# Kernel optimization log

Measured on AMD Instinct MI355X. Metric: run time of the kernel, lower is better.

The kernel has to match this reference:

```python
import jax, jax.numpy as jnp
import numpy as np

B, L, H, E = 8, 1024, 8, 64
HIST = 512


def setup_inputs() -> dict:
    key = jax.random.key(0)
    ks = jax.random.split(key, 6)
    shp = (B, L, H, E)
    q, k, v, qd, kd, vd = (jax.random.normal(kk, shp, dtype=jnp.float32) for kk in ks)
    # DoubleTriangularCausalMask surrogate: strictly-upper-triangular causal mask (diagonal=1)
    attn_mask = jnp.triu(jnp.ones((L, L), dtype=bool), k=1)[None, None]  # (1,1,L,S)
    return {
        "queries": q, "keys": k, "values": v,
        "queries_drawn": qd, "keys_drawn": kd, "values_drawn": vd,
        "attn_mask": attn_mask, "history_len": HIST,
    }


def reference(queries, keys, values, queries_drawn, keys_drawn, values_drawn, attn_mask, history_len):
    # drawn_y=True branch of FullFixedTimeCausalConstructiveAttention with history_len set.
    B, L, H, E = queries.shape
    scale = 1.0 / float(np.sqrt(E))
    hist = history_len
    idx = jnp.arange(hist, L)

    # queries[:, hist:] = queries_drawn[:, hist:]
    q_eff = jnp.concatenate([queries[:, :hist], queries_drawn[:, hist:]], axis=1)

    scores = jnp.einsum('blhe,bshe->bhls', q_eff, keys)  # (B,H,L,S)
    # diagonal positions l>=hist use drawn keys: q_eff[l] . keys_drawn[l]
    diag_scores = jnp.einsum('blhe,blhe->bhl', q_eff[:, hist:], keys_drawn[:, hist:])
    scores = scores.at[:, :, idx, idx].set(diag_scores)

    scores = jnp.where(attn_mask, -jnp.inf, scores)
    A = jax.nn.softmax(scale * scores, axis=-1)  # (B,H,L,S); dropout rate 0 in eval

    # values substitution on the diagonal (l==s, l>=hist) is a rank-1 correction;
    # avoids materializing the torch (B,H,D,L,S) repeated tensor.
    V = jnp.einsum('bhls,bshd->blhd', A, values)
    diag_A = A[:, :, idx, idx]                      # (B,H,L-hist)
    delta = values_drawn[:, hist:] - values[:, hist:]  # (B,L-hist,H,D)
    V = V.at[:, hist:].add(jnp.transpose(diag_A, (0, 2, 1))[..., None] * delta)
    return V
```

## Files before the change

### kernel.cpp

```cpp
#include <hip/hip_runtime.h>

#define LL   1024
#define HH   8
#define EE   64
#define KSTR 72

#define SCALE2 0.18033688011112043f

typedef _Float16 f16;
typedef _Float16 v8h  __attribute__((ext_vector_type(8)));
typedef _Float16 h2   __attribute__((ext_vector_type(2)));
typedef float    v4f  __attribute__((ext_vector_type(4)));
typedef int      v2i  __attribute__((ext_vector_type(2)));

__device__ __forceinline__ float fexp2(float x) {
#if __has_builtin(__builtin_amdgcn_exp2f)
  return __builtin_amdgcn_exp2f(x);
#else
  return __expf(x * 0.6931471805599453f);
#endif
}

__device__ __forceinline__ h2 pkh2(float a, float b) {
#if __has_builtin(__builtin_amdgcn_cvt_pkrtz)
  return __builtin_bit_cast(h2, __builtin_amdgcn_cvt_pkrtz(a, b));
#else
  h2 r; r[0] = (f16)a; r[1] = (f16)b; return r;
#endif
}

__device__ __forceinline__ float red4max(float x) {
#if __has_builtin(__builtin_amdgcn_permlane16_swap) && __has_builtin(__builtin_amdgcn_permlane32_swap)
  int xi = __float_as_int(x);
  v2i a = __builtin_amdgcn_permlane16_swap(xi, xi, false, false);
  float m = fmaxf(__int_as_float(a.x), __int_as_float(a.y));
  int mi = __float_as_int(m);
  v2i b = __builtin_amdgcn_permlane32_swap(mi, mi, false, false);
  return fmaxf(__int_as_float(b.x), __int_as_float(b.y));
#else
  x = fmaxf(x, __shfl_xor(x, 16));
  return fmaxf(x, __shfl_xor(x, 32));
#endif
}

__device__ __forceinline__ float red4sum(float x) {
#if __has_builtin(__builtin_amdgcn_permlane16_swap) && __has_builtin(__builtin_amdgcn_permlane32_swap)
  int xi = __float_as_int(x);
  v2i a = __builtin_amdgcn_permlane16_swap(xi, xi, false, false);
  float s = __int_as_float(a.x) + __int_as_float(a.y);
  int si = __float_as_int(s);
  v2i b = __builtin_amdgcn_permlane32_swap(si, si, false, false);
  return __int_as_float(b.x) + __int_as_float(b.y);
#else
  x += __shfl_xor(x, 16);
  return x + __shfl_xor(x, 32);
#endif
}

__device__ __forceinline__ void load16f(const float* __restrict__ p, float* __restrict__ f) {
  const float4* p4 = reinterpret_cast<const float4*>(p);
  float4 a = p4[0], b = p4[1], c = p4[2], d = p4[3];
  f[0]=a.x;  f[1]=a.y;  f[2]=a.z;  f[3]=a.w;
  f[4]=b.x;  f[5]=b.y;  f[6]=b.z;  f[7]=b.w;
  f[8]=c.x;  f[9]=c.y;  f[10]=c.z; f[11]=c.w;
  f[12]=d.x; f[13]=d.y; f[14]=d.z; f[15]=d.w;
}

__device__ __forceinline__ void load8f(const float* __restrict__ p, float* __restrict__ f) {
  const float4* p4 = reinterpret_cast<const float4*>(p);
  float4 a = p4[0], b = p4[1];
  f[0]=a.x; f[1]=a.y; f[2]=a.z; f[3]=a.w;
  f[4]=b.x; f[5]=b.y; f[6]=b.z; f[7]=b.w;
}

struct TileState {
  v4f   o[4];
  float m, l, pd;
};

__device__ __forceinline__ void tile_update(
    TileState& st, const v8h* __restrict__ qf, bool dt, bool drawn,
    const f16* __restrict__ Ks, const f16* __restrict__ Vt,
    const float* __restrict__ zd,
    int w, int ln, int lq,
    const int* __restrict__ rk, const int* __restrict__ kb)
{
  v4f S[4];
#pragma unroll
  for (int nb = 0; nb < 4; ++nb) {
    const f16* krow = &Ks[rk[nb] * KSTR + 8 * lq];
    v8h k0 = *reinterpret_cast<const v8h*>(krow);
    v8h k1 = *reinterpret_cast<const v8h*>(krow + 32);
    v4f acc = (v4f){0.f, 0.f, 0.f, 0.f};
    acc = __builtin_amdgcn_mfma_f32_16x16x32_f16(k0, qf[0], acc, 0, 0, 0);
    acc = __builtin_amdgcn_mfma_f32_16x16x32_f16(k1, qf[1], acc, 0, 0, 0);
    S[nb] = acc;
  }

  float z[4][4];
#pragma unroll
  for (int nb = 0; nb < 4; ++nb)
#pragma unroll
    for (int r = 0; r < 4; ++r) z[nb][r] = S[nb][r] * SCALE2;

  const int qlocal = w * 16 + ln;
  if (dt) {
    const float zdq = drawn ? zd[qlocal] : 0.f;
#pragma unroll
    for (int nb = 0; nb < 4; ++nb) {
#pragma unroll
      for (int r = 0; r < 4; ++r) {
        const int kl = kb[nb] + r;
        if (kl > qlocal)                 z[nb][r] = -1e30f;
        else if (drawn && kl == qlocal)  z[nb][r] = zdq;
      }
    }
  }

  float a0 = fmaxf(fmaxf(z[0][0], z[0][1]), fmaxf(z[0][2], z[0][3]));
  float a1 = fmaxf(fmaxf(z[1][0], z[1][1]), fmaxf(z[1][2], z[1][3]));
  float a2 = fmaxf(fmaxf(z[2][0], z[2][1]), fmaxf(z[2][2], z[2][3]));
  float a3 = fmaxf(fmaxf(z[3][0], z[3][1]), fmaxf(z[3][2], z[3][3]));
  const float mx = red4max(fmaxf(fmaxf(a0, a1), fmaxf(a2, a3)));

  const float mn = fmaxf(st.m, mx);
  const float al = fexp2(st.m - mn);
  st.m = mn;

  float p[4][4], rsum = 0.f, pdl = 0.f;
#pragma unroll
  for (int nb = 0; nb < 4; ++nb) {
#pragma unroll
    for (int r = 0; r < 4; ++r) {
      const float pv = fexp2(z[nb][r] - mn);
      p[nb][r] = pv;
      rsum += pv;
      if (dt && drawn && (kb[nb] + r) == qlocal) pdl = pv;
    }
  }
  rsum = red4sum(rsum);
  if (dt && drawn) st.pd = red4sum(pdl);
  st.l = st.l * al + rsum;
#pragma unroll
  for (int nb = 0; nb < 4; ++nb)
#pragma unroll
    for (int r = 0; r < 4; ++r) st.o[nb][r] *= al;

  h2 wq[4][2];
#pragma unroll
  for (int nb = 0; nb < 4; ++nb) {
    wq[nb][0] = pkh2(p[nb][0], p[nb][1]);
    wq[nb][1] = pkh2(p[nb][2], p[nb][3]);
  }
  const bool swp = (lq & 1);
  union U8 { v8h v; h2 h[4]; } A0, A1;
  A0.h[0] = swp ? wq[1][0] : wq[0][0];
  A0.h[1] = swp ? wq[1][1] : wq[0][1];
  A0.h[2] = swp ? wq[0][0] : wq[1][0];
  A0.h[3] = swp ? wq[0][1] : wq[1][1];
  A1.h[0] = swp ? wq[3][0] : wq[2][0];
  A1.h[1] = swp ? wq[3][1] : wq[2][1];
  A1.h[2] = swp ? wq[2][0] : wq[3][0];
  A1.h[3] = swp ? wq[2][1] : wq[3][1];

#pragma unroll
  for (int nb = 0; nb < 4; ++nb) {
    const int d   = nb * 16 + ln;
    const int dsw = (d >> 3) & 7;
    const f16* vbase = &Vt[d * KSTR];
    v8h v0 = *reinterpret_cast<const v8h*>(vbase + (((lq    ) ^ dsw) & 7) * 8);
    v8h v1 = *reinterpret_cast<const v8h*>(vbase + (((lq + 4) ^ dsw) & 7) * 8);
    st.o[nb] = __builtin_amdgcn_mfma_f32_16x16x32_f16(v0, A0.v, st.o[nb], 0, 0, 0);
    st.o[nb] = __builtin_amdgcn_mfma_f32_16x16x32_f16(v1, A1.v, st.o[nb], 0, 0, 0);
  }
}

extern "C" __global__ __launch_bounds__(256, 4)
void ftcca_split(const float* __restrict__ Q,  const float* __restrict__ K,
                 const float* __restrict__ V,  const float* __restrict__ Qd,
                 const float* __restrict__ Kd, const float* __restrict__ Vd,
                 float* __restrict__ out)
{
  __shared__ f16   Ks[64 * KSTR];
  __shared__ f16   Vt[64 * KSTR];
  __shared__ float zdiag[64];

  const int bh  = blockIdx.x & 63;
  const int a   = blockIdx.x >> 6;
  const int qt  = 15 - a;
  const bool drawn = (qt >= 8);
  const int b   = bh >> 3, h = bh & 7;
  const int t   = threadIdx.x;
  const int w    = t >> 6;
  const int lane = t & 63;
  const int ln   = lane & 15;
  const int lq   = lane >> 4;
  const int rs   = t >> 2;
  const int es0  = (t & 3) * 16;
  const int vr0  = (t >> 3) * 2;
  const int vd0  = (t & 7) * 8;

  const size_t base = ((size_t)b * LL * HH + h) * EE;
  const int ROWF = HH * EE;

  const int q2 = ln >> 2;
  int rk[4], kb[4];
  rk[0] = ln + ((q2 + 1) >> 1) * 8;
  rk[1] = ln + 4 + (q2 >> 1) * 8;
  rk[2] = rk[0] + 32;
  rk[3] = rk[1] + 32;
  kb[0] = 4 * lq + ((lq + 1) >> 1) * 8;
  kb[1] = 4 * lq + 4 + (lq >> 1) * 8;
  kb[2] = kb[0] + 32;
  kb[3] = kb[1] + 32;

  if (drawn) {
    const int l = qt * 64 + rs;
    const float* qrow = Qd + base + (size_t)l * ROWF + es0;
    const float* krow = Kd + base + (size_t)l * ROWF + es0;
    float par = 0.f;
#pragma unroll
    for (int i = 0; i < 16; ++i) par += qrow[i] * krow[i];
    par += __shfl_xor(par, 1);
    par += __shfl_xor(par, 2);
    if ((t & 3) == 0) zdiag[rs] = SCALE2 * par;
  }

  const int rowt_q = w * 16 + ln;
  const float* qsrc = drawn ? Qd : Q;
  v8h qf[2];
  {
    const float* pq = qsrc + base + (size_t)(qt * 64 + rowt_q) * ROWF;
#pragma unroll
    for (int c = 0; c < 2; ++c) {
      const float* x = pq + 32 * c + 8 * lq;
#pragma unroll
      for (int j = 0; j < 8; ++j) qf[c][j] = (f16)x[j];
    }
  }

  TileState st;
#pragma unroll
  for (int nb = 0; nb < 4; ++nb) st.o[nb] = (v4f){0, 0, 0, 0};
  st.m = -1e30f; st.l = 0.f; st.pd = 0.f;

  float tk[16], tv[16];
  load16f(K + base + (size_t)rs * ROWF + es0, tk);
  load8f(V + base + (size_t)vr0 * ROWF + vd0, tv);
  load8f(V + base + (size_t)(vr0 + 1) * ROWF + vd0, tv + 8);

  for (int i = 0; i <= qt; ++i) {
    __syncthreads();
    {
      v8h k0, k1;
#pragma unroll
      for (int j = 0; j < 8; ++j) { k0[j] = (f16)tk[j]; k1[j] = (f16)tk[8 + j]; }
      v8h* kd0 = reinterpret_cast<v8h*>(&Ks[rs * KSTR + es0]);
      kd0[0] = k0;
      kd0[1] = k1;
      const int vswz = vr0 >> 3;
#pragma unroll
      for (int dd = 0; dd < 8; ++dd) {
        const int d  = vd0 + dd;
        const int ch = (vswz ^ (d >> 3)) & 7;
        h2 val; val[0] = (f16)tv[dd]; val[1] = (f16)tv[8 + dd];
        *reinterpret_cast<h2*>(&Vt[d * KSTR + ch * 8 + (vr0 & 7)]) = val;
      }
    }
    __syncthreads();

    if (i < qt) {
      const size_t r0 = (size_t)((i + 1) * 64);
      load16f(K + base + (r0 + rs) * ROWF + es0, tk);
      load8f(V + base + (r0 + vr0) * ROWF + vd0, tv);
      load8f(V + base + (r0 + vr0 + 1) * ROWF + vd0, tv + 8);
    }

    tile_update(st, qf, i == qt, drawn, Ks, Vt, zdiag, w, ln, lq, rk, kb);
  }

  const float inv = 1.f / st.l;
  const float pdinv = st.pd * inv;
  const int lrow = qt * 64 + w * 16 + ln;

#pragma unroll
  for (int nb = 0; nb < 4; ++nb) {
    const int d0 = nb * 16 + lq * 4;
    const size_t g = base + (size_t)lrow * ROWF + d0;
    float4 o4;
    o4.x = st.o[nb][0] * inv;
    o4.y = st.o[nb][1] * inv;
    o4.z = st.o[nb][2] * inv;
    o4.w = st.o[nb][3] * inv;
    if (drawn) {
      float4 vd4 = *reinterpret_cast<const float4*>(Vd + g);
      float4 v4  = *reinterpret_cast<const float4*>(V + g);
      o4.x += pdinv * (vd4.x - v4.x);
      o4.y += pdinv * (vd4.y - v4.y);
      o4.z += pdinv * (vd4.z - v4.z);
      o4.w += pdinv * (vd4.w - v4.w);
    }
    *reinterpret_cast<float4*>(out + g) = o4;
  }
}

extern "C" void kernel_launch(void* const* d_in, const int* in_sizes, int n_in,
                              void* d_out, int out_size, void* d_ws, size_t ws_size,
                              hipStream_t stream) {
  const float* q  = (const float*)d_in[0];
  const float* k  = (const float*)d_in[1];
  const float* v  = (const float*)d_in[2];
  const float* qd = (const float*)d_in[3];
  const float* kd = (const float*)d_in[4];
  const float* vd = (const float*)d_in[5];
  float* out = (float*)d_out;

  ftcca_split<<<dim3(1024), dim3(256), 0, stream>>>(q, k, v, qd, kd, vd, out);
}
```

Before: 155.5 us.

## Pair mirrored causal query tiles per block to share K/V staging

Each block now processes two query tiles, a drawn tile 15-a and a history tile a, so the total causal work per block is balanced. The K/V tiles loaded into shared memory are reused by both tiles, which halves global loads and conversions and halves the grid size. The register footprint roughly doubles, so launch bounds drop to 2 blocks per SM, which lowers occupancy and may limit latency hiding.

```diff
diff --git a/kernel.cpp b/kernel.cpp
--- a/kernel.cpp
+++ b/kernel.cpp
@@ -12,6 +12,8 @@
 typedef _Float16 h2   __attribute__((ext_vector_type(2)));
 typedef float    v4f  __attribute__((ext_vector_type(4)));
 typedef int      v2i  __attribute__((ext_vector_type(2)));
+
+union U8 { v8h v; h2 h[4]; };
 
 __device__ __forceinline__ float fexp2(float x) {
 #if __has_builtin(__builtin_amdgcn_exp2f)
@@ -78,34 +80,17 @@
   float m, l, pd;
 };
 
-__device__ __forceinline__ void tile_update(
-    TileState& st, const v8h* __restrict__ qf, bool dt, bool drawn,
-    const f16* __restrict__ Ks, const f16* __restrict__ Vt,
-    const float* __restrict__ zd,
-    int w, int ln, int lq,
-    const int* __restrict__ rk, const int* __restrict__ kb)
+__device__ __forceinline__ void softmax_pack(
+    TileState& st, const v4f* __restrict__ S, bool dt, bool drawn, float zdq,
+    int qlocal, const int* __restrict__ kb, int lq, U8& A0, U8& A1)
 {
-  v4f S[4];
-#pragma unroll
-  for (int nb = 0; nb < 4; ++nb) {
-    const f16* krow = &Ks[rk[nb] * KSTR + 8 * lq];
-    v8h k0 = *reinterpret_cast<const v8h*>(krow);
-    v8h k1 = *reinterpret_cast<const v8h*>(krow + 32);
-    v4f acc = (v4f){0.f, 0.f, 0.f, 0.f};
-    acc = __builtin_amdgcn_mfma_f32_16x16x32_f16(k0, qf[0], acc, 0, 0, 0);
-    acc = __builtin_amdgcn_mfma_f32_16x16x32_f16(k1, qf[1], acc, 0, 0, 0);
-    S[nb] = acc;
-  }
-
   float z[4][4];
 #pragma unroll
   for (int nb = 0; nb < 4; ++nb)
 #pragma unroll
     for (int r = 0; r < 4; ++r) z[nb][r] = S[nb][r] * SCALE2;
 
-  const int qlocal = w * 16 + ln;
   if (dt) {
-    const float zdq = drawn ? zd[qlocal] : 0.f;
 #pragma unroll
     for (int nb = 0; nb < 4; ++nb) {
 #pragma unroll
@@ -153,7 +138,6 @@
     wq[nb][1] = pkh2(p[nb][2], p[nb][3]);
   }
   const bool swp = (lq & 1);
-  union U8 { v8h v; h2 h[4]; } A0, A1;
   A0.h[0] = swp ? wq[1][0] : wq[0][0];
   A0.h[1] = swp ? wq[1][1] : wq[0][1];
   A0.h[2] = swp ? wq[0][0] : wq[1][0];
@@ -162,21 +146,10 @@
   A1.h[1] = swp ? wq[3][1] : wq[2][1];
   A1.h[2] = swp ? wq[2][0] : wq[3][0];
   A1.h[3] = swp ? wq[2][1] : wq[3][1];
-
-#pragma unroll
-  for (int nb = 0; nb < 4; ++nb) {
-    const int d   = nb * 16 + ln;
-    const int dsw = (d >> 3) & 7;
-    const f16* vbase = &Vt[d * KSTR];
-    v8h v0 = *reinterpret_cast<const v8h*>(vbase + (((lq    ) ^ dsw) & 7) * 8);
-    v8h v1 = *reinterpret_cast<const v8h*>(vbase + (((lq + 4) ^ dsw) & 7) * 8);
-    st.o[nb] = __builtin_amdgcn_mfma_f32_16x16x32_f16(v0, A0.v, st.o[nb], 0, 0, 0);
-    st.o[nb] = __builtin_amdgcn_mfma_f32_16x16x32_f16(v1, A1.v, st.o[nb], 0, 0, 0);
-  }
-}
-
-extern "C" __global__ __launch_bounds__(256, 4)
-void ftcca_split(const float* __restrict__ Q,  const float* __restrict__ K,
+}
+
+extern "C" __global__ __launch_bounds__(256, 2)
+void ftcca_pair2(const float* __restrict__ Q,  const float* __restrict__ K,
                  const float* __restrict__ V,  const float* __restrict__ Qd,
                  const float* __restrict__ Kd, const float* __restrict__ Vd,
                  float* __restrict__ out)
@@ -187,8 +160,8 @@
 
   const int bh  = blockIdx.x & 63;
   const int a   = blockIdx.x >> 6;
-  const int qt  = 15 - a;
-  const bool drawn = (qt >= 8);
+  const int qtA = 15 - a;
+  const int qtB = a;
   const int b   = bh >> 3, h = bh & 7;
   const int t   = threadIdx.x;
   const int w    = t >> 6;
@@ -214,8 +187,8 @@
   kb[2] = kb[0] + 32;
   kb[3] = kb[1] + 32;
 
-  if (drawn) {
-    const int l = qt * 64 + rs;
+  {
+    const int l = qtA * 64 + rs;
     const float* qrow = Qd + base + (size_t)l * ROWF + es0;
     const float* krow = Kd + base + (size_t)l * ROWF + es0;
     float par = 0.f;
@@ -227,29 +200,33 @@
   }
 
   const int rowt_q = w * 16 + ln;
-  const float* qsrc = drawn ? Qd : Q;
-  v8h qf[2];
+  v8h qfA[2], qfB[2];
   {
-    const float* pq = qsrc + base + (size_t)(qt * 64 + rowt_q) * ROWF;
+    const float* pa = Qd + base + (size_t)(qtA * 64 + rowt_q) * ROWF;
+    const float* pb = Q  + base + (size_t)(qtB * 64 + rowt_q) * ROWF;
 #pragma unroll
     for (int c = 0; c < 2; ++c) {
-      const float* x = pq + 32 * c + 8 * lq;
-#pragma unroll
-      for (int j = 0; j < 8; ++j) qf[c][j] = (f16)x[j];
-    }
-  }
-
-  TileState st;
-#pragma unroll
-  for (int nb = 0; nb < 4; ++nb) st.o[nb] = (v4f){0, 0, 0, 0};
-  st.m = -1e30f; st.l = 0.f; st.pd = 0.f;
+      const float* xa = pa + 32 * c + 8 * lq;
+      const float* xb = pb + 32 * c + 8 * lq;
+#pragma unroll
+      for (int j = 0; j < 8; ++j) { qfA[c][j] = (f16)xa[j]; qfB[c][j] = (f16)xb[j]; }
+    }
+  }
+
+  TileState stA, stB;
+#pragma unroll
+  for (int nb = 0; nb < 4; ++nb) { stA.o[nb] = (v4f){0,0,0,0}; stB.o[nb] = (v4f){0,0,0,0}; }
+  stA.m = -1e30f; stA.l = 0.f; stA.pd = 0.f;
+  stB.m = -1e30f; stB.l = 0.f; stB.pd = 0.f;
+
+  const int qlocal = w * 16 + ln;
 
   float tk[16], tv[16];
   load16f(K + base + (size_t)rs * ROWF + es0, tk);
   load8f(V + base + (size_t)vr0 * ROWF + vd0, tv);
   load8f(V + base + (size_t)(vr0 + 1) * ROWF + vd0, tv + 8);
 
-  for (int i = 0; i <= qt; ++i) {
+  for (int i = 0; i <= qtA; ++i) {
     __syncthreads();
     {
       v8h k0, k1;
@@ -269,38 +246,97 @@
     }
     __syncthreads();
 
-    if (i < qt) {
+    if (i < qtA) {
       const size_t r0 = (size_t)((i + 1) * 64);
       load16f(K + base + (r0 + rs) * ROWF + es0, tk);
       load8f(V + base + (r0 + vr0) * ROWF + vd0, tv);
       load8f(V + base + (r0 + vr0 + 1) * ROWF + vd0, tv + 8);
     }
 
-    tile_update(st, qf, i == qt, drawn, Ks, Vt, zdiag, w, ln, lq, rk, kb);
-  }
-
-  const float inv = 1.f / st.l;
-  const float pdinv = st.pd * inv;
-  const int lrow = qt * 64 + w * 16 + ln;
-
-#pragma unroll
-  for (int nb = 0; nb < 4; ++nb) {
-    const int d0 = nb * 16 + lq * 4;
-    const size_t g = base + (size_t)lrow * ROWF + d0;
-    float4 o4;
-    o4.x = st.o[nb][0] * inv;
-    o4.y = st.o[nb][1] * inv;
-    o4.z = st.o[nb][2] * inv;
-    o4.w = st.o[nb][3] * inv;
-    if (drawn) {
+    const bool doB = (i <= qtB);
+    const bool dtA = (i == qtA);
+    const bool dtB = (i == qtB);
+
+    v8h k0f[4], k1f[4];
+#pragma unroll
+    for (int nb = 0; nb < 4; ++nb) {
+      const f16* krow = &Ks[rk[nb] * KSTR + 8 * lq];
+      k0f[nb] = *reinterpret_cast<const v8h*>(krow);
+      k1f[nb] = *reinterpret_cast<const v8h*>(krow + 32);
+    }
+
+    v4f SA[4], SB[4];
+#pragma unroll
+    for (int nb = 0; nb < 4; ++nb) {
+      v4f acc = (v4f){0.f, 0.f, 0.f, 0.f};
+      acc = __builtin_amdgcn_mfma_f32_16x16x32_f16(k0f[nb], qfA[0], acc, 0, 0, 0);
+      acc = __builtin_amdgcn_mfma_f32_16x16x32_f16(k1f[nb], qfA[1], acc, 0, 0, 0);
+      SA[nb] = acc;
+    }
+    if (doB) {
+#pragma unroll
+      for (int nb = 0; nb < 4; ++nb) {
+        v4f acc = (v4f){0.f, 0.f, 0.f, 0.f};
+        acc = __builtin_amdgcn_mfma_f32_16x16x32_f16(k0f[nb], qfB[0], acc, 0, 0, 0);
+        acc = __builtin_amdgcn_mfma_f32_16x16x32_f16(k1f[nb], qfB[1], acc, 0, 0, 0);
+        SB[nb] = acc;
+      }
+    }
+
+    U8 pA0, pA1, pB0, pB1;
+    const float zdq = dtA ? zdiag[qlocal] : 0.f;
+    softmax_pack(stA, SA, dtA, true,  zdq, qlocal, kb, lq, pA0, pA1);
+    if (doB)
+      softmax_pack(stB, SB, dtB, false, 0.f, qlocal, kb, lq, pB0, pB1);
+
+#pragma unroll
+    for (int nb = 0; nb < 4; ++nb) {
+      const int d   = nb * 16 + ln;
+      const int dsw = (d >> 3) & 7;
+      const f16* vbase = &Vt[d * KSTR];
+      v8h v0 = *reinterpret_cast<const v8h*>(vbase + (((lq    ) ^ dsw) & 7) * 8);
+      v8h v1 = *reinterpret_cast<const v8h*>(vbase + (((lq + 4) ^ dsw) & 7) * 8);
+      stA.o[nb] = __builtin_amdgcn_mfma_f32_16x16x32_f16(v0, pA0.v, stA.o[nb], 0, 0, 0);
+      stA.o[nb] = __builtin_amdgcn_mfma_f32_16x16x32_f16(v1, pA1.v, stA.o[nb], 0, 0, 0);
+      if (doB) {
+        stB.o[nb] = __builtin_amdgcn_mfma_f32_16x16x32_f16(v0, pB0.v, stB.o[nb], 0, 0, 0);
+        stB.o[nb] = __builtin_amdgcn_mfma_f32_16x16x32_f16(v1, pB1.v, stB.o[nb], 0, 0, 0);
+      }
+    }
+  }
+
+  {
+    const float inv = 1.f / stA.l;
+    const float pdinv = stA.pd * inv;
+    const int lrow = qtA * 64 + w * 16 + ln;
+#pragma unroll
+    for (int nb = 0; nb < 4; ++nb) {
+      const int d0 = nb * 16 + lq * 4;
+      const size_t g = base + (size_t)lrow * ROWF + d0;
       float4 vd4 = *reinterpret_cast<const float4*>(Vd + g);
       float4 v4  = *reinterpret_cast<const float4*>(V + g);
-      o4.x += pdinv * (vd4.x - v4.x);
-      o4.y += pdinv * (vd4.y - v4.y);
-      o4.z += pdinv * (vd4.z - v4.z);
-      o4.w += pdinv * (vd4.w - v4.w);
-    }
-    *reinterpret_cast<float4*>(out + g) = o4;
+      float4 o4;
+      o4.x = stA.o[nb][0] * inv + pdinv * (vd4.x - v4.x);
+      o4.y = stA.o[nb][1] * inv + pdinv * (vd4.y - v4.y);
+      o4.z = stA.o[nb][2] * inv + pdinv * (vd4.z - v4.z);
+      o4.w = stA.o[nb][3] * inv + pdinv * (vd4.w - v4.w);
+      *reinterpret_cast<float4*>(out + g) = o4;
+    }
+  }
+  {
+    const float inv = 1.f / stB.l;
+    const int lrow = qtB * 64 + w * 16 + ln;
+#pragma unroll
+    for (int nb = 0; nb < 4; ++nb) {
+      const int d0 = nb * 16 + lq * 4;
+      const size_t g = base + (size_t)lrow * ROWF + d0;
+      float4 o4;
+      o4.x = stB.o[nb][0] * inv;
+      o4.y = stB.o[nb][1] * inv;
+      o4.z = stB.o[nb][2] * inv;
+      o4.w = stB.o[nb][3] * inv;
+      *reinterpret_cast<float4*>(out + g) = o4;
+    }
   }
 }
 
@@ -315,5 +351,5 @@
   const float* vd = (const float*)d_in[5];
   float* out = (float*)d_out;
 
-  ftcca_split<<<dim3(1024), dim3(256), 0, stream>>>(q, k, v, qd, kd, vd, out);
-}
+  ftcca_pair2<<<dim3(512), dim3(256), 0, stream>>>(q, k, v, qd, kd, vd, out);
+}
```

Measured after the change: 151.0 us. 1.03x faster.

## Double-buffer K/V shared-memory tiles to halve barriers per iteration

Applied to the files above, without the earlier changes.

Splits the K and V LDS tiles into two buffers. Each iteration writes the next tile into the alternate buffer while computing on the current one, so only one __syncthreads is needed per iteration instead of two, and the global prefetch runs two tiles ahead. This doubles LDS use per block (about 37KB), which may limit occupancy under launch_bounds(256,4), and keeps the prefetch registers live during compute.

```diff
diff --git a/kernel.cpp b/kernel.cpp
--- a/kernel.cpp
+++ b/kernel.cpp
@@ -176,13 +176,13 @@
 }
 
 extern "C" __global__ __launch_bounds__(256, 4)
-void ftcca_split(const float* __restrict__ Q,  const float* __restrict__ K,
-                 const float* __restrict__ V,  const float* __restrict__ Qd,
-                 const float* __restrict__ Kd, const float* __restrict__ Vd,
-                 float* __restrict__ out)
+void ftcca_dbuf(const float* __restrict__ Q,  const float* __restrict__ K,
+                const float* __restrict__ V,  const float* __restrict__ Qd,
+                const float* __restrict__ Kd, const float* __restrict__ Vd,
+                float* __restrict__ out)
 {
-  __shared__ f16   Ks[64 * KSTR];
-  __shared__ f16   Vt[64 * KSTR];
+  __shared__ f16   Ks[2][64 * KSTR];
+  __shared__ f16   Vt[2][64 * KSTR];
   __shared__ float zdiag[64];
 
   const int bh  = blockIdx.x & 63;
@@ -244,39 +244,63 @@
   for (int nb = 0; nb < 4; ++nb) st.o[nb] = (v4f){0, 0, 0, 0};
   st.m = -1e30f; st.l = 0.f; st.pd = 0.f;
 
+  const int iters = qt + 1;
+  const int vswz = vr0 >> 3;
+
   float tk[16], tv[16];
   load16f(K + base + (size_t)rs * ROWF + es0, tk);
   load8f(V + base + (size_t)vr0 * ROWF + vd0, tv);
   load8f(V + base + (size_t)(vr0 + 1) * ROWF + vd0, tv + 8);
-
-  for (int i = 0; i <= qt; ++i) {
-    __syncthreads();
-    {
+  {
+    v8h k0, k1;
+#pragma unroll
+    for (int j = 0; j < 8; ++j) { k0[j] = (f16)tk[j]; k1[j] = (f16)tk[8 + j]; }
+    v8h* kd0 = reinterpret_cast<v8h*>(&Ks[0][rs * KSTR + es0]);
+    kd0[0] = k0;
+    kd0[1] = k1;
+#pragma unroll
+    for (int dd = 0; dd < 8; ++dd) {
+      const int d  = vd0 + dd;
+      const int ch = (vswz ^ (d >> 3)) & 7;
+      h2 val; val[0] = (f16)tv[dd]; val[1] = (f16)tv[8 + dd];
+      *reinterpret_cast<h2*>(&Vt[0][d * KSTR + ch * 8 + (vr0 & 7)]) = val;
+    }
+  }
+  if (iters > 1) {
+    const size_t r0 = 64;
+    load16f(K + base + (r0 + rs) * ROWF + es0, tk);
+    load8f(V + base + (r0 + vr0) * ROWF + vd0, tv);
+    load8f(V + base + (r0 + vr0 + 1) * ROWF + vd0, tv + 8);
+  }
+  __syncthreads();
+
+  for (int i = 0; i < iters; ++i) {
+    if (i + 1 < iters) {
+      f16* Kw = Ks[(i + 1) & 1];
+      f16* Vw = Vt[(i + 1) & 1];
       v8h k0, k1;
 #pragma unroll
       for (int j = 0; j < 8; ++j) { k0[j] = (f16)tk[j]; k1[j] = (f16)tk[8 + j]; }
-      v8h* kd0 = reinterpret_cast<v8h*>(&Ks[rs * KSTR + es0]);
+      v8h* kd0 = reinterpret_cast<v8h*>(&Kw[rs * KSTR + es0]);
       kd0[0] = k0;
       kd0[1] = k1;
-      const int vswz = vr0 >> 3;
 #pragma unroll
       for (int dd = 0; dd < 8; ++dd) {
         const int d  = vd0 + dd;
         const int ch = (vswz ^ (d >> 3)) & 7;
         h2 val; val[0] = (f16)tv[dd]; val[1] = (f16)tv[8 + dd];
-        *reinterpret_cast<h2*>(&Vt[d * KSTR + ch * 8 + (vr0 & 7)]) = val;
+        *reinterpret_cast<h2*>(&Vw[d * KSTR + ch * 8 + (vr0 & 7)]) = val;
       }
-    }
+      if (i + 2 < iters) {
+        const size_t r0 = (size_t)((i + 2) * 64);
+        load16f(K + base + (r0 + rs) * ROWF + es0, tk);
+        load8f(V + base + (r0 + vr0) * ROWF + vd0, tv);
+        load8f(V + base + (r0 + vr0 + 1) * ROWF + vd0, tv + 8);
+      }
+    }
+
+    tile_update(st, qf, i == qt, drawn, Ks[i & 1], Vt[i & 1], zdiag, w, ln, lq, rk, kb);
     __syncthreads();
-
-    if (i < qt) {
-      const size_t r0 = (size_t)((i + 1) * 64);
-      load16f(K + base + (r0 + rs) * ROWF + es0, tk);
-      load8f(V + base + (r0 + vr0) * ROWF + vd0, tv);
-      load8f(V + base + (r0 + vr0 + 1) * ROWF + vd0, tv + 8);
-    }
-
-    tile_update(st, qf, i == qt, drawn, Ks, Vt, zdiag, w, ln, lq, rk, kb);
   }
 
   const float inv = 1.f / st.l;
@@ -315,5 +339,5 @@
   const float* vd = (const float*)d_in[5];
   float* out = (float*)d_out;
 
-  ftcca_split<<<dim3(1024), dim3(256), 0, stream>>>(q, k, v, qd, kd, vd, out);
-}
+  ftcca_dbuf<<<dim3(1024), dim3(256), 0, stream>>>(q, k, v, qd, kd, vd, out);
+}
```

Measured after the change: 157.5 us. About the same (+1.3%).

## Drop shared-memory staging; load K/V fragments directly from global memory per wave

Applied to the files above, without the earlier changes.

Removes the LDS tiles for K and transposed V along with the two barriers per iteration. Each wave now reads its MFMA K and V fragments straight from global memory and converts them to fp16 in registers. The diagonal drawn score is computed per lane with a cross-lane reduction instead of through shared memory. This trades barrier and LDS overhead for four-fold redundant global/L2 traffic across the waves of a block, strided scalar V loads, and the loss of software prefetch.

```diff
diff --git a/kernel.cpp b/kernel.cpp
--- a/kernel.cpp
+++ b/kernel.cpp
@@ -3,7 +3,6 @@
 #define LL   1024
 #define HH   8
 #define EE   64
-#define KSTR 72
 
 #define SCALE2 0.18033688011112043f
 
@@ -73,118 +72,12 @@
   f[4]=b.x; f[5]=b.y; f[6]=b.z; f[7]=b.w;
 }
 
-struct TileState {
-  v4f   o[4];
-  float m, l, pd;
-};
-
-__device__ __forceinline__ void tile_update(
-    TileState& st, const v8h* __restrict__ qf, bool dt, bool drawn,
-    const f16* __restrict__ Ks, const f16* __restrict__ Vt,
-    const float* __restrict__ zd,
-    int w, int ln, int lq,
-    const int* __restrict__ rk, const int* __restrict__ kb)
-{
-  v4f S[4];
-#pragma unroll
-  for (int nb = 0; nb < 4; ++nb) {
-    const f16* krow = &Ks[rk[nb] * KSTR + 8 * lq];
-    v8h k0 = *reinterpret_cast<const v8h*>(krow);
-    v8h k1 = *reinterpret_cast<const v8h*>(krow + 32);
-    v4f acc = (v4f){0.f, 0.f, 0.f, 0.f};
-    acc = __builtin_amdgcn_mfma_f32_16x16x32_f16(k0, qf[0], acc, 0, 0, 0);
-    acc = __builtin_amdgcn_mfma_f32_16x16x32_f16(k1, qf[1], acc, 0, 0, 0);
-    S[nb] = acc;
-  }
-
-  float z[4][4];
-#pragma unroll
-  for (int nb = 0; nb < 4; ++nb)
-#pragma unroll
-    for (int r = 0; r < 4; ++r) z[nb][r] = S[nb][r] * SCALE2;
-
-  const int qlocal = w * 16 + ln;
-  if (dt) {
-    const float zdq = drawn ? zd[qlocal] : 0.f;
-#pragma unroll
-    for (int nb = 0; nb < 4; ++nb) {
-#pragma unroll
-      for (int r = 0; r < 4; ++r) {
-        const int kl = kb[nb] + r;
-        if (kl > qlocal)                 z[nb][r] = -1e30f;
-        else if (drawn && kl == qlocal)  z[nb][r] = zdq;
-      }
-    }
-  }
-
-  float a0 = fmaxf(fmaxf(z[0][0], z[0][1]), fmaxf(z[0][2], z[0][3]));
-  float a1 = fmaxf(fmaxf(z[1][0], z[1][1]), fmaxf(z[1][2], z[1][3]));
-  float a2 = fmaxf(fmaxf(z[2][0], z[2][1]), fmaxf(z[2][2], z[2][3]));
-  float a3 = fmaxf(fmaxf(z[3][0], z[3][1]), fmaxf(z[3][2], z[3][3]));
-  const float mx = red4max(fmaxf(fmaxf(a0, a1), fmaxf(a2, a3)));
-
-  const float mn = fmaxf(st.m, mx);
-  const float al = fexp2(st.m - mn);
-  st.m = mn;
-
-  float p[4][4], rsum = 0.f, pdl = 0.f;
-#pragma unroll
-  for (int nb = 0; nb < 4; ++nb) {
-#pragma unroll
-    for (int r = 0; r < 4; ++r) {
-      const float pv = fexp2(z[nb][r] - mn);
-      p[nb][r] = pv;
-      rsum += pv;
-      if (dt && drawn && (kb[nb] + r) == qlocal) pdl = pv;
-    }
-  }
-  rsum = red4sum(rsum);
-  if (dt && drawn) st.pd = red4sum(pdl);
-  st.l = st.l * al + rsum;
-#pragma unroll
-  for (int nb = 0; nb < 4; ++nb)
-#pragma unroll
-    for (int r = 0; r < 4; ++r) st.o[nb][r] *= al;
-
-  h2 wq[4][2];
-#pragma unroll
-  for (int nb = 0; nb < 4; ++nb) {
-    wq[nb][0] = pkh2(p[nb][0], p[nb][1]);
-    wq[nb][1] = pkh2(p[nb][2], p[nb][3]);
-  }
-  const bool swp = (lq & 1);
-  union U8 { v8h v; h2 h[4]; } A0, A1;
-  A0.h[0] = swp ? wq[1][0] : wq[0][0];
-  A0.h[1] = swp ? wq[1][1] : wq[0][1];
-  A0.h[2] = swp ? wq[0][0] : wq[1][0];
-  A0.h[3] = swp ? wq[0][1] : wq[1][1];
-  A1.h[0] = swp ? wq[3][0] : wq[2][0];
-  A1.h[1] = swp ? wq[3][1] : wq[2][1];
-  A1.h[2] = swp ? wq[2][0] : wq[3][0];
-  A1.h[3] = swp ? wq[2][1] : wq[3][1];
-
-#pragma unroll
-  for (int nb = 0; nb < 4; ++nb) {
-    const int d   = nb * 16 + ln;
-    const int dsw = (d >> 3) & 7;
-    const f16* vbase = &Vt[d * KSTR];
-    v8h v0 = *reinterpret_cast<const v8h*>(vbase + (((lq    ) ^ dsw) & 7) * 8);
-    v8h v1 = *reinterpret_cast<const v8h*>(vbase + (((lq + 4) ^ dsw) & 7) * 8);
-    st.o[nb] = __builtin_amdgcn_mfma_f32_16x16x32_f16(v0, A0.v, st.o[nb], 0, 0, 0);
-    st.o[nb] = __builtin_amdgcn_mfma_f32_16x16x32_f16(v1, A1.v, st.o[nb], 0, 0, 0);
-  }
-}
-
-extern "C" __global__ __launch_bounds__(256, 4)
-void ftcca_split(const float* __restrict__ Q,  const float* __restrict__ K,
+extern "C" __global__ __launch_bounds__(256)
+void ftcca_nolds(const float* __restrict__ Q,  const float* __restrict__ K,
                  const float* __restrict__ V,  const float* __restrict__ Qd,
                  const float* __restrict__ Kd, const float* __restrict__ Vd,
                  float* __restrict__ out)
 {
-  __shared__ f16   Ks[64 * KSTR];
-  __shared__ f16   Vt[64 * KSTR];
-  __shared__ float zdiag[64];
-
   const int bh  = blockIdx.x & 63;
   const int a   = blockIdx.x >> 6;
   const int qt  = 15 - a;
@@ -195,10 +88,6 @@
   const int lane = t & 63;
   const int ln   = lane & 15;
   const int lq   = lane >> 4;
-  const int rs   = t >> 2;
-  const int es0  = (t & 3) * 16;
-  const int vr0  = (t >> 3) * 2;
-  const int vd0  = (t & 7) * 8;
 
   const size_t base = ((size_t)b * LL * HH + h) * EE;
   const int ROWF = HH * EE;
@@ -214,84 +103,159 @@
   kb[2] = kb[0] + 32;
   kb[3] = kb[1] + 32;
 
+  const int qlocal = w * 16 + ln;
+
+  float zdq = 0.f;
   if (drawn) {
-    const int l = qt * 64 + rs;
-    const float* qrow = Qd + base + (size_t)l * ROWF + es0;
-    const float* krow = Kd + base + (size_t)l * ROWF + es0;
-    float par = 0.f;
-#pragma unroll
-    for (int i = 0; i < 16; ++i) par += qrow[i] * krow[i];
-    par += __shfl_xor(par, 1);
-    par += __shfl_xor(par, 2);
-    if ((t & 3) == 0) zdiag[rs] = SCALE2 * par;
-  }
-
-  const int rowt_q = w * 16 + ln;
+    const int qrow = qt * 64 + qlocal;
+    float fq[16], fk[16];
+    load16f(Qd + base + (size_t)qrow * ROWF + 16 * lq, fq);
+    load16f(Kd + base + (size_t)qrow * ROWF + 16 * lq, fk);
+    float pa = 0.f;
+#pragma unroll
+    for (int ii = 0; ii < 16; ++ii) pa += fq[ii] * fk[ii];
+    zdq = SCALE2 * red4sum(pa);
+  }
+
   const float* qsrc = drawn ? Qd : Q;
   v8h qf[2];
   {
-    const float* pq = qsrc + base + (size_t)(qt * 64 + rowt_q) * ROWF;
+    const float* pq = qsrc + base + (size_t)(qt * 64 + qlocal) * ROWF;
 #pragma unroll
     for (int c = 0; c < 2; ++c) {
-      const float* x = pq + 32 * c + 8 * lq;
+      float x[8];
+      load8f(pq + 32 * c + 8 * lq, x);
 #pragma unroll
       for (int j = 0; j < 8; ++j) qf[c][j] = (f16)x[j];
     }
   }
 
-  TileState st;
-#pragma unroll
-  for (int nb = 0; nb < 4; ++nb) st.o[nb] = (v4f){0, 0, 0, 0};
-  st.m = -1e30f; st.l = 0.f; st.pd = 0.f;
-
-  float tk[16], tv[16];
-  load16f(K + base + (size_t)rs * ROWF + es0, tk);
-  load8f(V + base + (size_t)vr0 * ROWF + vd0, tv);
-  load8f(V + base + (size_t)(vr0 + 1) * ROWF + vd0, tv + 8);
+  v4f   o[4];
+#pragma unroll
+  for (int nb = 0; nb < 4; ++nb) o[nb] = (v4f){0, 0, 0, 0};
+  float m = -1e30f, l = 0.f, pd = 0.f;
 
   for (int i = 0; i <= qt; ++i) {
-    __syncthreads();
-    {
-      v8h k0, k1;
-#pragma unroll
-      for (int j = 0; j < 8; ++j) { k0[j] = (f16)tk[j]; k1[j] = (f16)tk[8 + j]; }
-      v8h* kd0 = reinterpret_cast<v8h*>(&Ks[rs * KSTR + es0]);
-      kd0[0] = k0;
-      kd0[1] = k1;
-      const int vswz = vr0 >> 3;
-#pragma unroll
-      for (int dd = 0; dd < 8; ++dd) {
-        const int d  = vd0 + dd;
-        const int ch = (vswz ^ (d >> 3)) & 7;
-        h2 val; val[0] = (f16)tv[dd]; val[1] = (f16)tv[8 + dd];
-        *reinterpret_cast<h2*>(&Vt[d * KSTR + ch * 8 + (vr0 & 7)]) = val;
+    const int kbase = i * 64;
+    const bool dt = (i == qt);
+
+    v8h k0f[4], k1f[4];
+#pragma unroll
+    for (int nb = 0; nb < 4; ++nb) {
+      const float* kr = K + base + (size_t)(kbase + rk[nb]) * ROWF;
+      float x0[8], x1[8];
+      load8f(kr + 8 * lq, x0);
+      load8f(kr + 32 + 8 * lq, x1);
+#pragma unroll
+      for (int j = 0; j < 8; ++j) { k0f[nb][j] = (f16)x0[j]; k1f[nb][j] = (f16)x1[j]; }
+    }
+
+    v4f S[4];
+#pragma unroll
+    for (int nb = 0; nb < 4; ++nb) {
+      v4f acc = (v4f){0.f, 0.f, 0.f, 0.f};
+      acc = __builtin_amdgcn_mfma_f32_16x16x32_f16(k0f[nb], qf[0], acc, 0, 0, 0);
+      acc = __builtin_amdgcn_mfma_f32_16x16x32_f16(k1f[nb], qf[1], acc, 0, 0, 0);
+      S[nb] = acc;
+    }
+
+    v8h vf0[4], vf1[4];
+#pragma unroll
+    for (int nb = 0; nb < 4; ++nb) {
+      const float* vc = V + base + (size_t)(kbase + 8 * lq) * ROWF + 16 * nb + ln;
+      float y0[8], y1[8];
+#pragma unroll
+      for (int j = 0; j < 8; ++j) y0[j] = vc[(size_t)j * ROWF];
+#pragma unroll
+      for (int j = 0; j < 8; ++j) y1[j] = vc[(size_t)(32 + j) * ROWF];
+#pragma unroll
+      for (int j = 0; j < 8; ++j) { vf0[nb][j] = (f16)y0[j]; vf1[nb][j] = (f16)y1[j]; }
+    }
+
+    float z[4][4];
+#pragma unroll
+    for (int nb = 0; nb < 4; ++nb)
+#pragma unroll
+      for (int r = 0; r < 4; ++r) z[nb][r] = S[nb][r] * SCALE2;
+
+    if (dt) {
+#pragma unroll
+      for (int nb = 0; nb < 4; ++nb) {
+#pragma unroll
+        for (int r = 0; r < 4; ++r) {
+          const int kl = kb[nb] + r;
+          if (kl > qlocal)                 z[nb][r] = -1e30f;
+          else if (drawn && kl == qlocal)  z[nb][r] = zdq;
+        }
       }
     }
-    __syncthreads();
-
-    if (i < qt) {
-      const size_t r0 = (size_t)((i + 1) * 64);
-      load16f(K + base + (r0 + rs) * ROWF + es0, tk);
-      load8f(V + base + (r0 + vr0) * ROWF + vd0, tv);
-      load8f(V + base + (r0 + vr0 + 1) * ROWF + vd0, tv + 8);
-    }
-
-    tile_update(st, qf, i == qt, drawn, Ks, Vt, zdiag, w, ln, lq, rk, kb);
-  }
-
-  const float inv = 1.f / st.l;
-  const float pdinv = st.pd * inv;
-  const int lrow = qt * 64 + w * 16 + ln;
+
+    float a0 = fmaxf(fmaxf(z[0][0], z[0][1]), fmaxf(z[0][2], z[0][3]));
+    float a1 = fmaxf(fmaxf(z[1][0], z[1][1]), fmaxf(z[1][2], z[1][3]));
+    float a2 = fmaxf(fmaxf(z[2][0], z[2][1]), fmaxf(z[2][2], z[2][3]));
+    float a3 = fmaxf(fmaxf(z[3][0], z[3][1]), fmaxf(z[3][2], z[3][3]));
+    const float mx = red4max(fmaxf(fmaxf(a0, a1), fmaxf(a2, a3)));
+
+    const float mn = fmaxf(m, mx);
+    const float al = fexp2(m - mn);
+    m = mn;
+
+    float p[4][4], rsum = 0.f, pdl = 0.f;
+#pragma unroll
+    for (int nb = 0; nb < 4; ++nb) {
+#pragma unroll
+      for (int r = 0; r < 4; ++r) {
+        const float pv = fexp2(z[nb][r] - mn);
+        p[nb][r] = pv;
+        rsum += pv;
+        if (dt && drawn && (kb[nb] + r) == qlocal) pdl = pv;
+      }
+    }
+    rsum = red4sum(rsum);
+    if (dt && drawn) pd = red4sum(pdl);
+    l = l * al + rsum;
+#pragma unroll
+    for (int nb = 0; nb < 4; ++nb)
+#pragma unroll
+      for (int r = 0; r < 4; ++r) o[nb][r] *= al;
+
+    h2 wq[4][2];
+#pragma unroll
+    for (int nb = 0; nb < 4; ++nb) {
+      wq[nb][0] = pkh2(p[nb][0], p[nb][1]);
+      wq[nb][1] = pkh2(p[nb][2], p[nb][3]);
+    }
+    const bool swp = (lq & 1);
+    union U8 { v8h v; h2 h[4]; } A0, A1;
+    A0.h[0] = swp ? wq[1][0] : wq[0][0];
+    A0.h[1] = swp ? wq[1][1] : wq[0][1];
+    A0.h[2] = swp ? wq[0][0] : wq[1][0];
+    A0.h[3] = swp ? wq[0][1] : wq[1][1];
+    A1.h[0] = swp ? wq[3][0] : wq[2][0];
+    A1.h[1] = swp ? wq[3][1] : wq[2][1];
+    A1.h[2] = swp ? wq[2][0] : wq[3][0];
+    A1.h[3] = swp ? wq[2][1] : wq[3][1];
+
+#pragma unroll
+    for (int nb = 0; nb < 4; ++nb) {
+      o[nb] = __builtin_amdgcn_mfma_f32_16x16x32_f16(vf0[nb], A0.v, o[nb], 0, 0, 0);
+      o[nb] = __builtin_amdgcn_mfma_f32_16x16x32_f16(vf1[nb], A1.v, o[nb], 0, 0, 0);
+    }
+  }
+
+  const float inv = 1.f / l;
+  const float pdinv = pd * inv;
+  const int lrow = qt * 64 + qlocal;
 
 #pragma unroll
   for (int nb = 0; nb < 4; ++nb) {
     const int d0 = nb * 16 + lq * 4;
     const size_t g = base + (size_t)lrow * ROWF + d0;
     float4 o4;
-    o4.x = st.o[nb][0] * inv;
-    o4.y = st.o[nb][1] * inv;
-    o4.z = st.o[nb][2] * inv;
-    o4.w = st.o[nb][3] * inv;
+    o4.x = o[nb][0] * inv;
+    o4.y = o[nb][1] * inv;
+    o4.z = o[nb][2] * inv;
+    o4.w = o[nb][3] * inv;
     if (drawn) {
       float4 vd4 = *reinterpret_cast<const float4*>(Vd + g);
       float4 v4  = *reinterpret_cast<const float4*>(V + g);
@@ -315,5 +279,5 @@
   const float* vd = (const float*)d_in[5];
   float* out = (float*)d_out;
 
-  ftcca_split<<<dim3(1024), dim3(256), 0, stream>>>(q, k, v, qd, kd, vd, out);
-}
+  ftcca_nolds<<<dim3(1024), dim3(256), 0, stream>>>(q, k, v, qd, kd, vd, out);
+}
```

After: 217.8 us. +40.1%, slower.
